# Performance work log

Measured on AMD Instinct MI355X. Metric: run time of the kernel, lower is better.

## Reference

```python
import jax, jax.numpy as jnp
import numpy as np

# Constants matching init_kwargs
N_HEADS = 8
D_MODEL = 256
PATCH_NUM = 128
D_K = D_MODEL // N_HEADS  # 32
TEMP = 0.5
EPS = 1e-10


def setup_inputs() -> dict:
    key = jax.random.key(0)
    ks = jax.random.split(key, 20)
    s = 0.02
    d, h, n = D_MODEL, N_HEADS, PATCH_NUM
    inp = {
        "x": jax.random.normal(ks[0], (32, n, d), dtype=jnp.float32),
        "gumbel_u": jax.random.uniform(ks[1], (h, n, n, 2), dtype=jnp.float32),
        "memory_w": jax.random.normal(ks[2], (n, h * d), dtype=jnp.float32) * s,
        "fc_out_w": jax.random.normal(ks[3], (2 * d, d), dtype=jnp.float32) * s,
        "fc_out_b": jnp.zeros((d,), jnp.float32),
        "fc_cat_w": jax.random.normal(ks[4], (d, 2), dtype=jnp.float32) * s,
        "fc_cat_b": jnp.zeros((2,), jnp.float32),
        "wq": jax.random.normal(ks[5], (d, d), dtype=jnp.float32) * s,
        "bq": jnp.zeros((d,), jnp.float32),
        "wk": jax.random.normal(ks[6], (d, d), dtype=jnp.float32) * s,
        "bk": jnp.zeros((d,), jnp.float32),
        "wv": jax.random.normal(ks[7], (d, d), dtype=jnp.float32) * s,
        "bv": jnp.zeros((d,), jnp.float32),
        "out_w": jax.random.normal(ks[8], (d, d), dtype=jnp.float32) * s,
        "out_b": jnp.zeros((d,), jnp.float32),
        "mlp_w1": jax.random.normal(ks[9], (d, d), dtype=jnp.float32) * s,
        "mlp_b1": jnp.zeros((d,), jnp.float32),
        "mlp_w2": jax.random.normal(ks[10], (d, d), dtype=jnp.float32) * s,
        "mlp_b2": jnp.zeros((d,), jnp.float32),
    }
    return inp


def _forward(x, memory_w, fc_out_w, fc_out_b, fc_cat_w, fc_cat_b,
             wq, bq, wk, bk, wv, bv, out_w, out_b,
             mlp_w1, mlp_b1, mlp_w2, mlp_b2, gumbel_u):
    H, N, D = N_HEADS, PATCH_NUM, D_MODEL
    B = x.shape[0]

    # ---- SSConnectionLearning on memory feats ----
    # memory: Embedding(N, d_model*n_heads) -> feats [H, N, D]
    feats = memory_w.reshape(N, H, D).transpose(1, 0, 2)
    # rel_rec gathers row index i (receiver), rel_send gathers col index j (sender)
    senders = jnp.broadcast_to(feats[:, None, :, :], (H, N, N, D))   # feats[j]
    receivers = jnp.broadcast_to(feats[:, :, None, :], (H, N, N, D))  # feats[i]
    pair = jnp.concatenate([senders, receivers], axis=-1)  # [H,N,N,2D]
    hdn = jax.nn.relu(jnp.einsum('hijc,cd->hijd', pair, fc_out_w) + fc_out_b)
    logits = jnp.einsum('hijd,dk->hijk', hdn, fc_cat_w) + fc_cat_b  # [H,N,N,2]

    # gumbel-softmax, hard=True, straight-through
    g = -jnp.log(-jnp.log(gumbel_u + EPS) + EPS)
    y_soft = jax.nn.softmax((logits + g) / TEMP, axis=-1)
    y_hard = jax.nn.one_hot(jnp.argmax(y_soft, axis=-1), 2, dtype=y_soft.dtype)
    y = jax.lax.stop_gradient(y_hard - y_soft) + y_soft
    conn = y[..., 1]  # [H,N,N] learned sparse connection mask

    # ---- PatchIntegration (GELU MLP, dropout = identity in eval) ----
    xm = jax.nn.gelu(x @ mlp_w1 + mlp_b1)
    xm = xm @ mlp_w2 + mlp_b2

    # ---- Multihead attention masked by connection matrix ----
    q = (xm @ wq + bq).reshape(B, N, H, D_K).transpose(0, 2, 1, 3)  # [B,H,N,dk]
    k = (xm @ wk + bk).reshape(B, N, H, D_K).transpose(0, 2, 1, 3)
    v = (xm @ wv + bv).reshape(B, N, H, D_K).transpose(0, 2, 1, 3)
    scale = D_K ** -0.5
    scores = jnp.einsum('bhqd,bhkd->bhqk', q, k) * scale
    # additive mask: blocked where conn==0 (large negative keeps softmax finite)
    scores = scores + (conn[None] - 1.0) * 1e9
    attn = jax.nn.softmax(scores, axis=-1)
    out = jnp.einsum('bhqk,bhkd->bhqd', attn, v)
    out = out.transpose(0, 2, 1, 3).reshape(B, N, H * D_K)
    out = out @ out_w + out_b
    return out


def reference(x, gumbel_u, memory_w, fc_out_w, fc_out_b, fc_cat_w, fc_cat_b,
              wq, bq, wk, bk, wv, bv, out_w, out_b,
              mlp_w1, mlp_b1, mlp_w2, mlp_b2):
    return _forward(x, memory_w, fc_out_w, fc_out_b, fc_cat_w, fc_cat_b,
                    wq, bq, wk, bk, wv, bv, out_w, out_b,
                    mlp_w1, mlp_b1, mlp_w2, mlp_b2, gumbel_u)
```

## Files before the change

kernel.cpp:

```cpp
#include <hip/hip_runtime.h>
#include <hip/hip_bf16.h>
#include <math.h>


typedef short short8 __attribute__((ext_vector_type(8)));
typedef float f32x4 __attribute__((ext_vector_type(4)));

union V8 { uint4 u; short8 s; };

__device__ __forceinline__ float gelu_f(float x) {
    float inner = 0.7978845608028654f * (x + 0.044715f * x * x * x);
    return 0.5f * x * (1.0f + tanhf(inner));
}
__device__ __forceinline__ void split_bf16(float x, ushort& h, ushort& l) {
    __hip_bfloat16 bh = __float2bfloat16(x);
    float hf = __bfloat162float(bh);
    __hip_bfloat16 bl = __float2bfloat16(x - hf);
    h = __builtin_bit_cast(ushort, bh);
    l = __builtin_bit_cast(ushort, bl);
}
__device__ __forceinline__ ushort bf16bits(float x) {
    return __builtin_bit_cast(ushort, __float2bfloat16(x));
}
__device__ __forceinline__ float bits_to_f(ushort v) {
    return __builtin_bit_cast(float, ((uint)v) << 16);
}
__device__ __forceinline__ short8 lds_frag(const ushort* p) {
    V8 v; v.u = *(const uint4*)p; return v.s;
}

__global__ __launch_bounds__(256) void k_wprep(
    const float* __restrict__ w0, const float* __restrict__ w1,
    const float* __restrict__ w2, const float* __restrict__ w3,
    const float* __restrict__ w4, const float* __restrict__ w5,
    const float* __restrict__ w6, const float* __restrict__ w7,
    ushort* __restrict__ hi, ushort* __restrict__ lo) {
    int bx = blockIdx.x;
    int m = bx >> 4, ks = (bx >> 1) & 7, nh = bx & 1;
    const float* W = m == 0 ? w0 : m == 1 ? w1 : m == 2 ? w2 : m == 3 ? w3 :
                     m == 4 ? w4 : m == 5 ? w5 : m == 6 ? w6 : w7;
    ushort* Hm = hi + m * 65536;
    ushort* Lm = lo + m * 65536;
    __shared__ __align__(16) float xs[32 * 132];
    int t = threadIdx.x;
    #pragma unroll
    for (int p = 0; p < 4; ++p) {
        int idx = p * 256 + t;
        int row = idx >> 5, c4 = (idx & 31) * 4;
        *(float4*)(xs + row * 132 + c4) =
            *(const float4*)(W + (ks * 32 + row) * 256 + nh * 128 + c4);
    }
    __syncthreads();
    int lane = t & 63, lr = lane & 15, quad = lane >> 4;
    #pragma unroll
    for (int it = 0; it < 2; ++it) {
        int tgl = (t >> 6) + 4 * it;
        int tg = nh * 8 + tgl;
        int nl = tgl * 16 + lr;
        ushort hb[8], lb[8];
        #pragma unroll
        for (int j = 0; j < 8; ++j)
            split_bf16(xs[(quad * 8 + j) * 132 + nl], hb[j], lb[j]);
        uint4 ph = { (uint)hb[0] | ((uint)hb[1] << 16), (uint)hb[2] | ((uint)hb[3] << 16),
                     (uint)hb[4] | ((uint)hb[5] << 16), (uint)hb[6] | ((uint)hb[7] << 16) };
        uint4 pl = { (uint)lb[0] | ((uint)lb[1] << 16), (uint)lb[2] | ((uint)lb[3] << 16),
                     (uint)lb[4] | ((uint)lb[5] << 16), (uint)lb[6] | ((uint)lb[7] << 16) };
        int idx = ((tg * 8 + ks) * 64 + lane) * 8;
        *(uint4*)(Hm + idx) = ph;
        *(uint4*)(Lm + idx) = pl;
    }
}

__global__ __launch_bounds__(256) void k_featproj(
    const float* __restrict__ memory_w,
    const ushort* __restrict__ Whi, const ushort* __restrict__ Wlo,
    float* __restrict__ A, float* __restrict__ Bm) {
    __shared__ __align__(16) ushort xhi[16 * 264], xlo[16 * 264];
    int t = threadIdx.x;
    int rt = blockIdx.x;
    int msel = blockIdx.y & 1, cq = blockIdx.y >> 1;
    #pragma unroll
    for (int ii = 0; ii < 4; ++ii) {
        int f4 = ii * 256 + t;
        int rr = f4 >> 6, c = (f4 & 63) * 4;
        int r = rt * 16 + rr;
        int h = r >> 7, n = r & 127;
        float4 xv = *(const float4*)(memory_w + n * 2048 + h * 256 + c);
        ushort hh[4], ll[4];
        split_bf16(xv.x, hh[0], ll[0]); split_bf16(xv.y, hh[1], ll[1]);
        split_bf16(xv.z, hh[2], ll[2]); split_bf16(xv.w, hh[3], ll[3]);
        uint2 ph = { (uint)hh[0] | ((uint)hh[1] << 16), (uint)hh[2] | ((uint)hh[3] << 16) };
        uint2 pl = { (uint)ll[0] | ((uint)ll[1] << 16), (uint)ll[2] | ((uint)ll[3] << 16) };
        *(uint2*)(xhi + rr * 264 + c) = ph;
        *(uint2*)(xlo + rr * 264 + c) = pl;
    }
    __syncthreads();
    int l = t & 63, w = t >> 6;
    int lr = l & 15, quad = l >> 4;
    int tg = cq * 4 + w;
    const uint4* H4 = (const uint4*)(Whi + (6 + msel) * 65536);
    const uint4* L4 = (const uint4*)(Wlo + (6 + msel) * 65536);
    const ushort* ah = xhi + lr * 264 + quad * 8;
    const ushort* al = xlo + lr * 264 + quad * 8;
    f32x4 acc = {};
    #pragma unroll
    for (int ks = 0; ks < 8; ++ks) {
        short8 a_h = lds_frag(ah + ks * 32);
        short8 a_l = lds_frag(al + ks * 32);
        int off = (tg * 8 + ks) * 64 + l;
        V8 bh, bl; bh.u = H4[off]; bl.u = L4[off];
        acc = __builtin_amdgcn_mfma_f32_16x16x32_bf16(a_h, bh.s, acc, 0, 0, 0);
        acc = __builtin_amdgcn_mfma_f32_16x16x32_bf16(a_l, bh.s, acc, 0, 0, 0);
        acc = __builtin_amdgcn_mfma_f32_16x16x32_bf16(a_h, bl.s, acc, 0, 0, 0);
    }
    float* O = msel ? Bm : A;
    int n0 = tg * 16 + lr;
    #pragma unroll
    for (int r = 0; r < 4; ++r)
        O[(rt * 16 + quad * 4 + r) * 256 + n0] = acc[r];
}

__global__ __launch_bounds__(256) void k_conn(
    const float* __restrict__ A, const float* __restrict__ Bm,
    const float* __restrict__ fc_out_b, const float* __restrict__ fc_cat_w,
    const float* __restrict__ fc_cat_b, const float* __restrict__ gumbel_u,
    ushort* __restrict__ maskb) {
    int bx = blockIdx.x;
    int h = bx >> 6, it = (bx >> 3) & 7, jt = bx & 7;
    int i0 = it * 16, j0 = jt * 16;
    int t = threadIdx.x;
    int il = t >> 4, jl = t & 15;
    __shared__ __align__(16) float sA[16 * 260], sB[16 * 260];
    #pragma unroll
    for (int p = 0; p < 4; ++p) {
        int idx = p * 256 + t;
        int rr = idx >> 6, c = (idx & 63) * 4;
        *(float4*)(sA + rr * 260 + c) =
            *(const float4*)(A + (h * 128 + j0 + rr) * 256 + c);
        float4 bv = *(const float4*)(Bm + (h * 128 + i0 + rr) * 256 + c);
        float4 fb = *(const float4*)(fc_out_b + c);
        bv.x += fb.x; bv.y += fb.y; bv.z += fb.z; bv.w += fb.w;
        *(float4*)(sB + rr * 260 + c) = bv;
    }
    __syncthreads();
    const float* Ar = sA + jl * 260;
    const float* Br = sB + il * 260;
    float l0 = fc_cat_b[0], l1 = fc_cat_b[1];
    #pragma unroll 4
    for (int d4 = 0; d4 < 64; ++d4) {
        int d = d4 * 4;
        float4 av = *(const float4*)(Ar + d);
        float4 bv = *(const float4*)(Br + d);
        float4 cwA = *(const float4*)(fc_cat_w + d * 2);
        float4 cwB = *(const float4*)(fc_cat_w + d * 2 + 4);
        float h0 = fmaxf(av.x + bv.x, 0.f);
        float h1 = fmaxf(av.y + bv.y, 0.f);
        float h2 = fmaxf(av.z + bv.z, 0.f);
        float h3 = fmaxf(av.w + bv.w, 0.f);
        l0 += h0 * cwA.x + h1 * cwA.z + h2 * cwB.x + h3 * cwB.z;
        l1 += h0 * cwA.y + h1 * cwA.w + h2 * cwB.y + h3 * cwB.w;
    }
    int i = i0 + il, j = j0 + jl;
    float2 uu = *(const float2*)(gumbel_u + ((h * 128 + i) * 128 + j) * 2);
    float g0 = -logf(-logf(uu.x + 1e-10f) + 1e-10f);
    float g1 = -logf(-logf(uu.y + 1e-10f) + 1e-10f);
    bool on = (l1 + g1) > (l0 + g0);
    maskb[(h * 128 + i) * 128 + j] = bf16bits(on ? 0.f : -1e9f);
}

__global__ __launch_bounds__(512) void k_fused3(
    const float* __restrict__ X,
    const ushort* __restrict__ Whi, const ushort* __restrict__ Wlo,
    const float* __restrict__ b1, const float* __restrict__ b2,
    const float* __restrict__ Bq, const float* __restrict__ Bk,
    const float* __restrict__ Bv,
    ushort* __restrict__ Q, ushort* __restrict__ K, ushort* __restrict__ V) {
    __shared__ __align__(16) ushort aHi[16 * 264], aLo[16 * 264];
    __shared__ __align__(16) ushort bHi[16 * 264], bLo[16 * 264];
    int t = threadIdx.x;
    int r0 = blockIdx.x * 16;
    #pragma unroll
    for (int ii = 0; ii < 2; ++ii) {
        int f4 = ii * 512 + t;
        int row = f4 >> 6, c = (f4 & 63) * 4;
        float4 xv = *(const float4*)(X + (r0 + row) * 256 + c);
        ushort h[4], l[4];
        split_bf16(xv.x, h[0], l[0]); split_bf16(xv.y, h[1], l[1]);
        split_bf16(xv.z, h[2], l[2]); split_bf16(xv.w, h[3], l[3]);
        uint2 ph = { (uint)h[0] | ((uint)h[1] << 16), (uint)h[2] | ((uint)h[3] << 16) };
        uint2 pl = { (uint)l[0] | ((uint)l[1] << 16), (uint)l[2] | ((uint)l[3] << 16) };
        *(uint2*)(aHi + row * 264 + c) = ph;
        *(uint2*)(aLo + row * 264 + c) = pl;
    }
    __syncthreads();
    int lane = t & 63, w = t >> 6;
    int lr = lane & 15, quad = lane >> 4;
    int aoff = lr * 264 + quad * 8;
    {
        const uint4* H4 = (const uint4*)(Whi + 0 * 65536);
        const uint4* L4 = (const uint4*)(Wlo + 0 * 65536);
        f32x4 acc[2] = {};
        #pragma unroll
        for (int ks = 0; ks < 8; ++ks) {
            short8 a_h = lds_frag(aHi + aoff + ks * 32);
            short8 a_l = lds_frag(aLo + aoff + ks * 32);
            #pragma unroll
            for (int ti = 0; ti < 2; ++ti) {
                int off = ((w * 2 + ti) * 8 + ks) * 64 + lane;
                V8 bh, bl; bh.u = H4[off]; bl.u = L4[off];
                acc[ti] = __builtin_amdgcn_mfma_f32_16x16x32_bf16(a_h, bh.s, acc[ti], 0, 0, 0);
                acc[ti] = __builtin_amdgcn_mfma_f32_16x16x32_bf16(a_l, bh.s, acc[ti], 0, 0, 0);
                acc[ti] = __builtin_amdgcn_mfma_f32_16x16x32_bf16(a_h, bl.s, acc[ti], 0, 0, 0);
            }
        }
        #pragma unroll
        for (int ti = 0; ti < 2; ++ti) {
            int n0 = (w * 2 + ti) * 16 + lr;
            float bb = b1[n0];
            #pragma unroll
            for (int r = 0; r < 4; ++r) {
                float o = gelu_f(acc[ti][r] + bb);
                ushort hh, ll; split_bf16(o, hh, ll);
                int ad = (quad * 4 + r) * 264 + n0;
                bHi[ad] = hh; bLo[ad] = ll;
            }
        }
    }
    __syncthreads();
    {
        const uint4* H4 = (const uint4*)(Whi + 1 * 65536);
        const uint4* L4 = (const uint4*)(Wlo + 1 * 65536);
        f32x4 acc[2] = {};
        #pragma unroll
        for (int ks = 0; ks < 8; ++ks) {
            short8 a_h = lds_frag(bHi + aoff + ks * 32);
            short8 a_l = lds_frag(bLo + aoff + ks * 32);
            #pragma unroll
            for (int ti = 0; ti < 2; ++ti) {
                int off = ((w * 2 + ti) * 8 + ks) * 64 + lane;
                V8 bh, bl; bh.u = H4[off]; bl.u = L4[off];
                acc[ti] = __builtin_amdgcn_mfma_f32_16x16x32_bf16(a_h, bh.s, acc[ti], 0, 0, 0);
                acc[ti] = __builtin_amdgcn_mfma_f32_16x16x32_bf16(a_l, bh.s, acc[ti], 0, 0, 0);
                acc[ti] = __builtin_amdgcn_mfma_f32_16x16x32_bf16(a_h, bl.s, acc[ti], 0, 0, 0);
            }
        }
        __syncthreads();
        #pragma unroll
        for (int ti = 0; ti < 2; ++ti) {
            int n0 = (w * 2 + ti) * 16 + lr;
            float bb = b2[n0];
            #pragma unroll
            for (int r = 0; r < 4; ++r) {
                float o = acc[ti][r] + bb;
                ushort hh, ll; split_bf16(o, hh, ll);
                int ad = (quad * 4 + r) * 264 + n0;
                aHi[ad] = hh; aLo[ad] = ll;
            }
        }
    }
    __syncthreads();
    {
        const uint4* Hq = (const uint4*)(Whi + 2 * 65536);
        const uint4* Lq = (const uint4*)(Wlo + 2 * 65536);
        const uint4* Hk = (const uint4*)(Whi + 3 * 65536);
        const uint4* Lk = (const uint4*)(Wlo + 3 * 65536);
        const uint4* Hv = (const uint4*)(Whi + 4 * 65536);
        const uint4* Lv = (const uint4*)(Wlo + 4 * 65536);
        f32x4 aq[2] = {}, ak[2] = {}, av[2] = {};
        #pragma unroll 2
        for (int ks = 0; ks < 8; ++ks) {
            short8 a_h = lds_frag(aHi + aoff + ks * 32);
            short8 a_l = lds_frag(aLo + aoff + ks * 32);
            #pragma unroll
            for (int ti = 0; ti < 2; ++ti) {
                int off = ((w * 2 + ti) * 8 + ks) * 64 + lane;
                V8 qh, ql, kh, kl, vh, vl;
                qh.u = Hq[off]; ql.u = Lq[off];
                kh.u = Hk[off]; kl.u = Lk[off];
                vh.u = Hv[off]; vl.u = Lv[off];
                aq[ti] = __builtin_amdgcn_mfma_f32_16x16x32_bf16(a_h, qh.s, aq[ti], 0, 0, 0);
                aq[ti] = __builtin_amdgcn_mfma_f32_16x16x32_bf16(a_l, qh.s, aq[ti], 0, 0, 0);
                aq[ti] = __builtin_amdgcn_mfma_f32_16x16x32_bf16(a_h, ql.s, aq[ti], 0, 0, 0);
                ak[ti] = __builtin_amdgcn_mfma_f32_16x16x32_bf16(a_h, kh.s, ak[ti], 0, 0, 0);
                ak[ti] = __builtin_amdgcn_mfma_f32_16x16x32_bf16(a_l, kh.s, ak[ti], 0, 0, 0);
                ak[ti] = __builtin_amdgcn_mfma_f32_16x16x32_bf16(a_h, kl.s, ak[ti], 0, 0, 0);
                av[ti] = __builtin_amdgcn_mfma_f32_16x16x32_bf16(a_h, vh.s, av[ti], 0, 0, 0);
                av[ti] = __builtin_amdgcn_mfma_f32_16x16x32_bf16(a_l, vh.s, av[ti], 0, 0, 0);
                av[ti] = __builtin_amdgcn_mfma_f32_16x16x32_bf16(a_h, vl.s, av[ti], 0, 0, 0);
            }
        }
        #pragma unroll
        for (int ti = 0; ti < 2; ++ti) {
            int n0 = (w * 2 + ti) * 16 + lr;
            float bq = Bq[n0], bk = Bk[n0], bv = Bv[n0];
            #pragma unroll
            for (int r = 0; r < 4; ++r) {
                int go = (r0 + quad * 4 + r) * 256 + n0;
                Q[go] = bf16bits(aq[ti][r] + bq);
                K[go] = bf16bits(ak[ti][r] + bk);
                V[go] = bf16bits(av[ti][r] + bv);
            }
        }
    }
}

__global__ __launch_bounds__(256) void k_attn_mfma(
    const ushort* __restrict__ Q, const ushort* __restrict__ K,
    const ushort* __restrict__ V, const ushort* __restrict__ maskb,
    float* __restrict__ AO) {
    int bx = blockIdx.x;
    int b = bx >> 4, h = (bx >> 1) & 7, rh = bx & 1;
    int t = threadIdx.x;
    int lane = t & 63, w = t >> 6;
    __shared__ __align__(16) ushort vT[32 * 136];
    __shared__ __align__(16) ushort ps[64 * 136];
    #pragma unroll
    for (int it = 0; it < 2; ++it) {
        int idx = it * 256 + t;
        int key = idx >> 2, dq8 = (idx & 3) * 8;
        V8 vv; vv.u = *(const uint4*)(V + (b * 128 + key) * 256 + h * 32 + dq8);
        #pragma unroll
        for (int m = 0; m < 8; ++m)
            vT[(dq8 + m) * 136 + key] = (ushort)vv.s[m];
    }
    __syncthreads();
    int lr = lane & 15, quad = lane >> 4;
    int rt = rh * 4 + w;
    V8 af;
    af.u = *(const uint4*)(Q + (b * 128 + rt * 16 + lr) * 256 + h * 32 + quad * 8);
    f32x4 s[8];
    #pragma unroll
    for (int ct = 0; ct < 8; ++ct) {
        V8 bf_;
        bf_.u = *(const uint4*)(K + (b * 128 + ct * 16 + lr) * 256 + h * 32 + quad * 8);
        f32x4 z = {0.f, 0.f, 0.f, 0.f};
        s[ct] = __builtin_amdgcn_mfma_f32_16x16x32_bf16(af.s, bf_.s, z, 0, 0, 0);
    }
    const float scale = 0.17677669529663687f;
    const ushort* mrow = maskb + h * 16384;
    #pragma unroll
    for (int r = 0; r < 4; ++r) {
        int lrow = w * 16 + quad * 4 + r;
        int grow = rt * 16 + quad * 4 + r;
        float sv[8];
        float mx = -3.0e38f;
        #pragma unroll
        for (int ct = 0; ct < 8; ++ct) {
            float bias = bits_to_f(mrow[grow * 128 + ct * 16 + lr]);
            sv[ct] = s[ct][r] * scale + bias;
            mx = fmaxf(mx, sv[ct]);
        }
        mx = fmaxf(mx, __shfl_xor(mx, 1));
        mx = fmaxf(mx, __shfl_xor(mx, 2));
        mx = fmaxf(mx, __shfl_xor(mx, 4));
        mx = fmaxf(mx, __shfl_xor(mx, 8));
        float sum = 0.f;
        #pragma unroll
        for (int ct = 0; ct < 8; ++ct) {
            sv[ct] = __expf(sv[ct] - mx);
            sum += sv[ct];
        }
        sum += __shfl_xor(sum, 1);
        sum += __shfl_xor(sum, 2);
        sum += __shfl_xor(sum, 4);
        sum += __shfl_xor(sum, 8);
        float iv = 1.f / sum;
        #pragma unroll
        for (int ct = 0; ct < 8; ++ct)
            ps[lrow * 136 + ct * 16 + lr] = bf16bits(sv[ct] * iv);
    }
    f32x4 o0 = {}, o1 = {};
    #pragma unroll
    for (int kk = 0; kk < 4; ++kk) {
        short8 pa = lds_frag(ps + (w * 16 + lr) * 136 + kk * 32 + quad * 8);
        short8 v0 = lds_frag(vT + lr * 136 + kk * 32 + quad * 8);
        short8 v1 = lds_frag(vT + (16 + lr) * 136 + kk * 32 + quad * 8);
        o0 = __builtin_amdgcn_mfma_f32_16x16x32_bf16(pa, v0, o0, 0, 0, 0);
        o1 = __builtin_amdgcn_mfma_f32_16x16x32_bf16(pa, v1, o1, 0, 0, 0);
    }
    #pragma unroll
    for (int r = 0; r < 4; ++r) {
        int grow = rt * 16 + quad * 4 + r;
        float* op = AO + b * 32768 + grow * 256 + h * 32;
        op[lr] = o0[r];
        op[16 + lr] = o1[r];
    }
}

__global__ __launch_bounds__(256) void k_gemm16(
    const float* __restrict__ X, const ushort* __restrict__ Whi,
    const ushort* __restrict__ Wlo, const float* __restrict__ bias,
    float* __restrict__ Y) {
    __shared__ __align__(16) ushort xhi[16 * 264], xlo[16 * 264];
    int t = threadIdx.x;
    int r0 = blockIdx.x * 16;
    #pragma unroll
    for (int ii = 0; ii < 4; ++ii) {
        int f4 = ii * 256 + t;
        int row = f4 >> 6, c = (f4 & 63) * 4;
        float4 xv = *(const float4*)(X + (r0 + row) * 256 + c);
        ushort h[4], l[4];
        split_bf16(xv.x, h[0], l[0]); split_bf16(xv.y, h[1], l[1]);
        split_bf16(xv.z, h[2], l[2]); split_bf16(xv.w, h[3], l[3]);
        uint2 ph = { (uint)h[0] | ((uint)h[1] << 16), (uint)h[2] | ((uint)h[3] << 16) };
        uint2 pl = { (uint)l[0] | ((uint)l[1] << 16), (uint)l[2] | ((uint)l[3] << 16) };
        *(uint2*)(xhi + row * 264 + c) = ph;
        *(uint2*)(xlo + row * 264 + c) = pl;
    }
    __syncthreads();
    int l = t & 63, w = t >> 6;
    int lr = l & 15, quad = l >> 4;
    int tg = blockIdx.y * 4 + w;
    const ushort* ah = xhi + lr * 264 + quad * 8;
    const ushort* al = xlo + lr * 264 + quad * 8;
    const uint4* H4 = (const uint4*)Whi;
    const uint4* L4 = (const uint4*)Wlo;
    f32x4 acc = {};
    #pragma unroll
    for (int ks = 0; ks < 8; ++ks) {
        short8 a_h = lds_frag(ah + ks * 32);
        short8 a_l = lds_frag(al + ks * 32);
        int off = (tg * 8 + ks) * 64 + l;
        V8 bh, bl; bh.u = H4[off]; bl.u = L4[off];
        acc = __builtin_amdgcn_mfma_f32_16x16x32_bf16(a_h, bh.s, acc, 0, 0, 0);
        acc = __builtin_amdgcn_mfma_f32_16x16x32_bf16(a_l, bh.s, acc, 0, 0, 0);
        acc = __builtin_amdgcn_mfma_f32_16x16x32_bf16(a_h, bl.s, acc, 0, 0, 0);
    }
    int n0 = tg * 16 + lr;
    float bs = bias[n0];
    #pragma unroll
    for (int r = 0; r < 4; ++r)
        Y[(r0 + quad * 4 + r) * 256 + n0] = acc[r] + bs;
}

extern "C" void kernel_launch(void* const* d_in, const int* in_sizes, int n_in,
                              void* d_out, int out_size, void* d_ws, size_t ws_size,
                              hipStream_t stream) {
    const float* x        = (const float*)d_in[0];
    const float* gumbel_u = (const float*)d_in[1];
    const float* memory_w = (const float*)d_in[2];
    const float* fc_out_w = (const float*)d_in[3];
    const float* fc_out_b = (const float*)d_in[4];
    const float* fc_cat_w = (const float*)d_in[5];
    const float* fc_cat_b = (const float*)d_in[6];
    const float* wq       = (const float*)d_in[7];
    const float* bq       = (const float*)d_in[8];
    const float* wk       = (const float*)d_in[9];
    const float* bk       = (const float*)d_in[10];
    const float* wv_      = (const float*)d_in[11];
    const float* bv_      = (const float*)d_in[12];
    const float* out_w    = (const float*)d_in[13];
    const float* out_b    = (const float*)d_in[14];
    const float* mlp_w1   = (const float*)d_in[15];
    const float* mlp_b1   = (const float*)d_in[16];
    const float* mlp_w2   = (const float*)d_in[17];
    const float* mlp_b2   = (const float*)d_in[18];

    float* ws    = (float*)d_ws;
    float* A     = ws;
    float* Bm    = ws + 262144;
    ushort* mask = (ushort*)(ws + 524288);
    ushort* qb   = (ushort*)(ws + 589824);
    ushort* kb   = (ushort*)(ws + 1114112);
    ushort* vb   = (ushort*)(ws + 1638400);
    float* ao    = ws + 2162688;
    ushort* wf_hi = (ushort*)(ws + 3211264);
    ushort* wf_lo = wf_hi + 8 * 65536;
    float* out   = (float*)d_out;

    k_wprep<<<dim3(128), dim3(256), 0, stream>>>(
        mlp_w1, mlp_w2, wq, wk, wv_, out_w, fc_out_w, fc_out_w + 65536,
        wf_hi, wf_lo);
    k_featproj<<<dim3(64, 8), dim3(256), 0, stream>>>(memory_w, wf_hi, wf_lo, A, Bm);
    k_fused3<<<dim3(256), dim3(512), 0, stream>>>(x, wf_hi, wf_lo, mlp_b1, mlp_b2,
                                                  bq, bk, bv_, qb, kb, vb);
    k_conn<<<dim3(512), dim3(256), 0, stream>>>(A, Bm, fc_out_b, fc_cat_w, fc_cat_b,
                                                gumbel_u, mask);
    k_attn_mfma<<<dim3(512), dim3(256), 0, stream>>>(qb, kb, vb, mask, ao);
    k_gemm16<<<dim3(256, 4), dim3(256), 0, stream>>>(ao, wf_hi + 5 * 65536,
                                                     wf_lo + 5 * 65536, out_b, out);
}
```

Baseline: 159.2 us.

## Merge feature projection and MLP/QKV kernels into one launch, widen blocks

Combines the memory-feature projection kernel and the fused MLP+QKV kernel into a single launch, with the block index choosing the work: 64 blocks do the feature projection and 256 blocks do the MLP+QKV path. This removes one kernel launch and lets the two independent stages run at the same time. The weight-prep and connection kernels switch to 512-thread blocks that each handle twice the work, halving their grid sizes. The risks are load imbalance between the two block types, since the feature blocks now loop over four column tiles each, and lower occupancy from the larger blocks.

New measurement: 144.7 us (median of 2 runs). 1.1x faster.

```diff
diff --git a/kernel.cpp b/kernel.cpp
--- a/kernel.cpp
+++ b/kernel.cpp
@@ -29,32 +29,36 @@
     V8 v; v.u = *(const uint4*)p; return v.s;
 }
 
-__global__ __launch_bounds__(256) void k_wprep(
-    const float* __restrict__ w0, const float* __restrict__ w1,
-    const float* __restrict__ w2, const float* __restrict__ w3,
-    const float* __restrict__ w4, const float* __restrict__ w5,
-    const float* __restrict__ w6, const float* __restrict__ w7,
+
+__global__ __launch_bounds__(512) void k_wprep(
+    const float* __restrict__ mlp_w1, const float* __restrict__ mlp_w2,
+    const float* __restrict__ wq, const float* __restrict__ wk,
+    const float* __restrict__ wv, const float* __restrict__ out_w,
+    const float* __restrict__ fc_out_w,
     ushort* __restrict__ hi, ushort* __restrict__ lo) {
-    int bx = blockIdx.x;
-    int m = bx >> 4, ks = (bx >> 1) & 7, nh = bx & 1;
-    const float* W = m == 0 ? w0 : m == 1 ? w1 : m == 2 ? w2 : m == 3 ? w3 :
-                     m == 4 ? w4 : m == 5 ? w5 : m == 6 ? w6 : w7;
+    __shared__ __align__(16) float xs2[2][32 * 132];
+    int bx = blockIdx.x, t = threadIdx.x;
+    int half = t >> 8, tl = t & 255;
+    int job = bx * 2 + half;
+    int m = job >> 4, ks = (job >> 1) & 7, nh = job & 1;
+    const float* W = m == 0 ? mlp_w1 : m == 1 ? mlp_w2 : m == 2 ? wq :
+                     m == 3 ? wk : m == 4 ? wv : m == 5 ? out_w :
+                     m == 6 ? fc_out_w : fc_out_w + 65536;
     ushort* Hm = hi + m * 65536;
     ushort* Lm = lo + m * 65536;
-    __shared__ __align__(16) float xs[32 * 132];
-    int t = threadIdx.x;
+    float* xs = xs2[half];
     #pragma unroll
     for (int p = 0; p < 4; ++p) {
-        int idx = p * 256 + t;
+        int idx = p * 256 + tl;
         int row = idx >> 5, c4 = (idx & 31) * 4;
         *(float4*)(xs + row * 132 + c4) =
             *(const float4*)(W + (ks * 32 + row) * 256 + nh * 128 + c4);
     }
     __syncthreads();
-    int lane = t & 63, lr = lane & 15, quad = lane >> 4;
+    int lane = tl & 63, lr = lane & 15, quad = lane >> 4;
     #pragma unroll
     for (int it = 0; it < 2; ++it) {
-        int tgl = (t >> 6) + 4 * it;
+        int tgl = (tl >> 6) + 4 * it;
         int tg = nh * 8 + tgl;
         int nl = tgl * 16 + lr;
         ushort hb[8], lb[8];
@@ -71,76 +75,222 @@
     }
 }
 
-__global__ __launch_bounds__(256) void k_featproj(
-    const float* __restrict__ memory_w,
+__global__ __launch_bounds__(512) void k_p2(
+    const float* __restrict__ memory_w, const float* __restrict__ X,
     const ushort* __restrict__ Whi, const ushort* __restrict__ Wlo,
-    float* __restrict__ A, float* __restrict__ Bm) {
-    __shared__ __align__(16) ushort xhi[16 * 264], xlo[16 * 264];
-    int t = threadIdx.x;
-    int rt = blockIdx.x;
-    int msel = blockIdx.y & 1, cq = blockIdx.y >> 1;
-    #pragma unroll
-    for (int ii = 0; ii < 4; ++ii) {
-        int f4 = ii * 256 + t;
-        int rr = f4 >> 6, c = (f4 & 63) * 4;
-        int r = rt * 16 + rr;
-        int h = r >> 7, n = r & 127;
-        float4 xv = *(const float4*)(memory_w + n * 2048 + h * 256 + c);
-        ushort hh[4], ll[4];
-        split_bf16(xv.x, hh[0], ll[0]); split_bf16(xv.y, hh[1], ll[1]);
-        split_bf16(xv.z, hh[2], ll[2]); split_bf16(xv.w, hh[3], ll[3]);
-        uint2 ph = { (uint)hh[0] | ((uint)hh[1] << 16), (uint)hh[2] | ((uint)hh[3] << 16) };
-        uint2 pl = { (uint)ll[0] | ((uint)ll[1] << 16), (uint)ll[2] | ((uint)ll[3] << 16) };
-        *(uint2*)(xhi + rr * 264 + c) = ph;
-        *(uint2*)(xlo + rr * 264 + c) = pl;
-    }
-    __syncthreads();
-    int l = t & 63, w = t >> 6;
-    int lr = l & 15, quad = l >> 4;
-    int tg = cq * 4 + w;
-    const uint4* H4 = (const uint4*)(Whi + (6 + msel) * 65536);
-    const uint4* L4 = (const uint4*)(Wlo + (6 + msel) * 65536);
-    const ushort* ah = xhi + lr * 264 + quad * 8;
-    const ushort* al = xlo + lr * 264 + quad * 8;
-    f32x4 acc = {};
-    #pragma unroll
-    for (int ks = 0; ks < 8; ++ks) {
-        short8 a_h = lds_frag(ah + ks * 32);
-        short8 a_l = lds_frag(al + ks * 32);
-        int off = (tg * 8 + ks) * 64 + l;
-        V8 bh, bl; bh.u = H4[off]; bl.u = L4[off];
-        acc = __builtin_amdgcn_mfma_f32_16x16x32_bf16(a_h, bh.s, acc, 0, 0, 0);
-        acc = __builtin_amdgcn_mfma_f32_16x16x32_bf16(a_l, bh.s, acc, 0, 0, 0);
-        acc = __builtin_amdgcn_mfma_f32_16x16x32_bf16(a_h, bl.s, acc, 0, 0, 0);
-    }
-    float* O = msel ? Bm : A;
-    int n0 = tg * 16 + lr;
-    #pragma unroll
-    for (int r = 0; r < 4; ++r)
-        O[(rt * 16 + quad * 4 + r) * 256 + n0] = acc[r];
-}
-
-__global__ __launch_bounds__(256) void k_conn(
-    const float* __restrict__ A, const float* __restrict__ Bm,
+    const float* __restrict__ b1, const float* __restrict__ b2,
+    const float* __restrict__ Bq, const float* __restrict__ Bk,
+    const float* __restrict__ Bv,
+    float* __restrict__ A, float* __restrict__ Bm,
+    ushort* __restrict__ Q, ushort* __restrict__ K, ushort* __restrict__ V) {
+    __shared__ __align__(16) union {
+        struct { ushort xhi[16 * 264], xlo[16 * 264]; } f;
+        struct {
+            ushort aHi[16 * 264], aLo[16 * 264];
+            ushort bHi[16 * 264], bLo[16 * 264];
+        } g;
+    } sm;
+    int bx = blockIdx.x, t = threadIdx.x;
+    if (bx < 64) {
+        int rt = bx;
+        #pragma unroll
+        for (int ii = 0; ii < 2; ++ii) {
+            int f4 = ii * 512 + t;
+            int rr = f4 >> 6, c = (f4 & 63) * 4;
+            int r = rt * 16 + rr;
+            int h = r >> 7, n = r & 127;
+            float4 xv = *(const float4*)(memory_w + n * 2048 + h * 256 + c);
+            ushort hh[4], ll[4];
+            split_bf16(xv.x, hh[0], ll[0]); split_bf16(xv.y, hh[1], ll[1]);
+            split_bf16(xv.z, hh[2], ll[2]); split_bf16(xv.w, hh[3], ll[3]);
+            uint2 ph = { (uint)hh[0] | ((uint)hh[1] << 16), (uint)hh[2] | ((uint)hh[3] << 16) };
+            uint2 pl = { (uint)ll[0] | ((uint)ll[1] << 16), (uint)ll[2] | ((uint)ll[3] << 16) };
+            *(uint2*)(sm.f.xhi + rr * 264 + c) = ph;
+            *(uint2*)(sm.f.xlo + rr * 264 + c) = pl;
+        }
+        __syncthreads();
+        int lane = t & 63, w = t >> 6;
+        int lr = lane & 15, quad = lane >> 4;
+        int msel = w & 1, cq = w >> 1;
+        const uint4* H4 = (const uint4*)(Whi + (6 + msel) * 65536);
+        const uint4* L4 = (const uint4*)(Wlo + (6 + msel) * 65536);
+        const ushort* ah = sm.f.xhi + lr * 264 + quad * 8;
+        const ushort* al = sm.f.xlo + lr * 264 + quad * 8;
+        float* O = msel ? Bm : A;
+        #pragma unroll
+        for (int i = 0; i < 4; ++i) {
+            int tg = cq * 4 + i;
+            f32x4 acc = {};
+            #pragma unroll
+            for (int ks = 0; ks < 8; ++ks) {
+                short8 a_h = lds_frag(ah + ks * 32);
+                short8 a_l = lds_frag(al + ks * 32);
+                int off = (tg * 8 + ks) * 64 + lane;
+                V8 bh, bl; bh.u = H4[off]; bl.u = L4[off];
+                acc = __builtin_amdgcn_mfma_f32_16x16x32_bf16(a_h, bh.s, acc, 0, 0, 0);
+                acc = __builtin_amdgcn_mfma_f32_16x16x32_bf16(a_l, bh.s, acc, 0, 0, 0);
+                acc = __builtin_amdgcn_mfma_f32_16x16x32_bf16(a_h, bl.s, acc, 0, 0, 0);
+            }
+            int n0 = tg * 16 + lr;
+            #pragma unroll
+            for (int r = 0; r < 4; ++r)
+                O[(rt * 16 + quad * 4 + r) * 256 + n0] = acc[r];
+        }
+        return;
+    }
+    int r0 = (bx - 64) * 16;
+    #pragma unroll
+    for (int ii = 0; ii < 2; ++ii) {
+        int f4 = ii * 512 + t;
+        int row = f4 >> 6, c = (f4 & 63) * 4;
+        float4 xv = *(const float4*)(X + (r0 + row) * 256 + c);
+        ushort h[4], l[4];
+        split_bf16(xv.x, h[0], l[0]); split_bf16(xv.y, h[1], l[1]);
+        split_bf16(xv.z, h[2], l[2]); split_bf16(xv.w, h[3], l[3]);
+        uint2 ph = { (uint)h[0] | ((uint)h[1] << 16), (uint)h[2] | ((uint)h[3] << 16) };
+        uint2 pl = { (uint)l[0] | ((uint)l[1] << 16), (uint)l[2] | ((uint)l[3] << 16) };
+        *(uint2*)(sm.g.aHi + row * 264 + c) = ph;
+        *(uint2*)(sm.g.aLo + row * 264 + c) = pl;
+    }
+    __syncthreads();
+    int lane = t & 63, w = t >> 6;
+    int lr = lane & 15, quad = lane >> 4;
+    int aoff = lr * 264 + quad * 8;
+    {
+        const uint4* H4 = (const uint4*)(Whi + 0 * 65536);
+        const uint4* L4 = (const uint4*)(Wlo + 0 * 65536);
+        f32x4 acc[2] = {};
+        #pragma unroll
+        for (int ks = 0; ks < 8; ++ks) {
+            short8 a_h = lds_frag(sm.g.aHi + aoff + ks * 32);
+            short8 a_l = lds_frag(sm.g.aLo + aoff + ks * 32);
+            #pragma unroll
+            for (int ti = 0; ti < 2; ++ti) {
+                int off = ((w * 2 + ti) * 8 + ks) * 64 + lane;
+                V8 bh, bl; bh.u = H4[off]; bl.u = L4[off];
+                acc[ti] = __builtin_amdgcn_mfma_f32_16x16x32_bf16(a_h, bh.s, acc[ti], 0, 0, 0);
+                acc[ti] = __builtin_amdgcn_mfma_f32_16x16x32_bf16(a_l, bh.s, acc[ti], 0, 0, 0);
+                acc[ti] = __builtin_amdgcn_mfma_f32_16x16x32_bf16(a_h, bl.s, acc[ti], 0, 0, 0);
+            }
+        }
+        #pragma unroll
+        for (int ti = 0; ti < 2; ++ti) {
+            int n0 = (w * 2 + ti) * 16 + lr;
+            float bb = b1[n0];
+            #pragma unroll
+            for (int r = 0; r < 4; ++r) {
+                float o = gelu_f(acc[ti][r] + bb);
+                ushort hh, ll; split_bf16(o, hh, ll);
+                int ad = (quad * 4 + r) * 264 + n0;
+                sm.g.bHi[ad] = hh; sm.g.bLo[ad] = ll;
+            }
+        }
+    }
+    __syncthreads();
+    {
+        const uint4* H4 = (const uint4*)(Whi + 1 * 65536);
+        const uint4* L4 = (const uint4*)(Wlo + 1 * 65536);
+        f32x4 acc[2] = {};
+        #pragma unroll
+        for (int ks = 0; ks < 8; ++ks) {
+            short8 a_h = lds_frag(sm.g.bHi + aoff + ks * 32);
+            short8 a_l = lds_frag(sm.g.bLo + aoff + ks * 32);
+            #pragma unroll
+            for (int ti = 0; ti < 2; ++ti) {
+                int off = ((w * 2 + ti) * 8 + ks) * 64 + lane;
+                V8 bh, bl; bh.u = H4[off]; bl.u = L4[off];
+                acc[ti] = __builtin_amdgcn_mfma_f32_16x16x32_bf16(a_h, bh.s, acc[ti], 0, 0, 0);
+                acc[ti] = __builtin_amdgcn_mfma_f32_16x16x32_bf16(a_l, bh.s, acc[ti], 0, 0, 0);
+                acc[ti] = __builtin_amdgcn_mfma_f32_16x16x32_bf16(a_h, bl.s, acc[ti], 0, 0, 0);
+            }
+        }
+        __syncthreads();
+        #pragma unroll
+        for (int ti = 0; ti < 2; ++ti) {
+            int n0 = (w * 2 + ti) * 16 + lr;
+            float bb = b2[n0];
+            #pragma unroll
+            for (int r = 0; r < 4; ++r) {
+                float o = acc[ti][r] + bb;
+                ushort hh, ll; split_bf16(o, hh, ll);
+                int ad = (quad * 4 + r) * 264 + n0;
+                sm.g.aHi[ad] = hh; sm.g.aLo[ad] = ll;
+            }
+        }
+    }
+    __syncthreads();
+    {
+        const uint4* Hq = (const uint4*)(Whi + 2 * 65536);
+        const uint4* Lq = (const uint4*)(Wlo + 2 * 65536);
+        const uint4* Hk = (const uint4*)(Whi + 3 * 65536);
+        const uint4* Lk = (const uint4*)(Wlo + 3 * 65536);
+        const uint4* Hv = (const uint4*)(Whi + 4 * 65536);
+        const uint4* Lv = (const uint4*)(Wlo + 4 * 65536);
+        f32x4 aq[2] = {}, ak[2] = {}, av[2] = {};
+        #pragma unroll 2
+        for (int ks = 0; ks < 8; ++ks) {
+            short8 a_h = lds_frag(sm.g.aHi + aoff + ks * 32);
+            short8 a_l = lds_frag(sm.g.aLo + aoff + ks * 32);
+            #pragma unroll
+            for (int ti = 0; ti < 2; ++ti) {
+                int off = ((w * 2 + ti) * 8 + ks) * 64 + lane;
+                V8 qh, ql, kh, kl, vh, vl;
+                qh.u = Hq[off]; ql.u = Lq[off];
+                kh.u = Hk[off]; kl.u = Lk[off];
+                vh.u = Hv[off]; vl.u = Lv[off];
+                aq[ti] = __builtin_amdgcn_mfma_f32_16x16x32_bf16(a_h, qh.s, aq[ti], 0, 0, 0);
+                aq[ti] = __builtin_amdgcn_mfma_f32_16x16x32_bf16(a_l, qh.s, aq[ti], 0, 0, 0);
+                aq[ti] = __builtin_amdgcn_mfma_f32_16x16x32_bf16(a_h, ql.s, aq[ti], 0, 0, 0);
+                ak[ti] = __builtin_amdgcn_mfma_f32_16x16x32_bf16(a_h, kh.s, ak[ti], 0, 0, 0);
+                ak[ti] = __builtin_amdgcn_mfma_f32_16x16x32_bf16(a_l, kh.s, ak[ti], 0, 0, 0);
+                ak[ti] = __builtin_amdgcn_mfma_f32_16x16x32_bf16(a_h, kl.s, ak[ti], 0, 0, 0);
+                av[ti] = __builtin_amdgcn_mfma_f32_16x16x32_bf16(a_h, vh.s, av[ti], 0, 0, 0);
+                av[ti] = __builtin_amdgcn_mfma_f32_16x16x32_bf16(a_l, vh.s, av[ti], 0, 0, 0);
+                av[ti] = __builtin_amdgcn_mfma_f32_16x16x32_bf16(a_h, vl.s, av[ti], 0, 0, 0);
+            }
+        }
+        #pragma unroll
+        for (int ti = 0; ti < 2; ++ti) {
+            int n0 = (w * 2 + ti) * 16 + lr;
+            float bq = Bq[n0], bk = Bk[n0], bv = Bv[n0];
+            #pragma unroll
+            for (int r = 0; r < 4; ++r) {
+                int go = (r0 + quad * 4 + r) * 256 + n0;
+                Q[go] = bf16bits(aq[ti][r] + bq);
+                K[go] = bf16bits(ak[ti][r] + bk);
+                V[go] = bf16bits(av[ti][r] + bv);
+            }
+        }
+    }
+}
+
+__global__ __launch_bounds__(512) void k_conn(
+    const float* __restrict__ A, const float* __restrict__ Bmat,
     const float* __restrict__ fc_out_b, const float* __restrict__ fc_cat_w,
     const float* __restrict__ fc_cat_b, const float* __restrict__ gumbel_u,
     ushort* __restrict__ maskb) {
-    int bx = blockIdx.x;
-    int h = bx >> 6, it = (bx >> 3) & 7, jt = bx & 7;
-    int i0 = it * 16, j0 = jt * 16;
-    int t = threadIdx.x;
-    int il = t >> 4, jl = t & 15;
-    __shared__ __align__(16) float sA[16 * 260], sB[16 * 260];
-    #pragma unroll
-    for (int p = 0; p < 4; ++p) {
-        int idx = p * 256 + t;
-        int rr = idx >> 6, c = (idx & 63) * 4;
-        *(float4*)(sA + rr * 260 + c) =
-            *(const float4*)(A + (h * 128 + j0 + rr) * 256 + c);
-        float4 bv = *(const float4*)(Bm + (h * 128 + i0 + rr) * 256 + c);
-        float4 fb = *(const float4*)(fc_out_b + c);
-        bv.x += fb.x; bv.y += fb.y; bv.z += fb.z; bv.w += fb.w;
-        *(float4*)(sB + rr * 260 + c) = bv;
+    __shared__ __align__(16) float sA[16 * 260], sB[32 * 260];
+    int bx = blockIdx.x, t = threadIdx.x;
+    int h = bx >> 5;
+    int rem = bx & 31;
+    int it = rem >> 3, jt = rem & 7;
+    int i0 = it * 32, j0 = jt * 16;
+    int jl = t & 15, il = t >> 4;
+    #pragma unroll
+    for (int p = 0; p < 6; ++p) {
+        int id2 = p * 512 + t;
+        if (id2 < 1024) {
+            int rr = id2 >> 6, c = (id2 & 63) * 4;
+            *(float4*)(sA + rr * 260 + c) =
+                *(const float4*)(A + (h * 128 + j0 + rr) * 256 + c);
+        } else {
+            int id3 = id2 - 1024;
+            int rr = id3 >> 6, c = (id3 & 63) * 4;
+            float4 bv = *(const float4*)(Bmat + (h * 128 + i0 + rr) * 256 + c);
+            float4 fb = *(const float4*)(fc_out_b + c);
+            bv.x += fb.x; bv.y += fb.y; bv.z += fb.z; bv.w += fb.w;
+            *(float4*)(sB + rr * 260 + c) = bv;
+        }
     }
     __syncthreads();
     const float* Ar = sA + jl * 260;
@@ -166,142 +316,6 @@
     float g1 = -logf(-logf(uu.y + 1e-10f) + 1e-10f);
     bool on = (l1 + g1) > (l0 + g0);
     maskb[(h * 128 + i) * 128 + j] = bf16bits(on ? 0.f : -1e9f);
-}
-
-__global__ __launch_bounds__(512) void k_fused3(
-    const float* __restrict__ X,
-    const ushort* __restrict__ Whi, const ushort* __restrict__ Wlo,
-    const float* __restrict__ b1, const float* __restrict__ b2,
-    const float* __restrict__ Bq, const float* __restrict__ Bk,
-    const float* __restrict__ Bv,
-    ushort* __restrict__ Q, ushort* __restrict__ K, ushort* __restrict__ V) {
-    __shared__ __align__(16) ushort aHi[16 * 264], aLo[16 * 264];
-    __shared__ __align__(16) ushort bHi[16 * 264], bLo[16 * 264];
-    int t = threadIdx.x;
-    int r0 = blockIdx.x * 16;
-    #pragma unroll
-    for (int ii = 0; ii < 2; ++ii) {
-        int f4 = ii * 512 + t;
-        int row = f4 >> 6, c = (f4 & 63) * 4;
-        float4 xv = *(const float4*)(X + (r0 + row) * 256 + c);
-        ushort h[4], l[4];
-        split_bf16(xv.x, h[0], l[0]); split_bf16(xv.y, h[1], l[1]);
-        split_bf16(xv.z, h[2], l[2]); split_bf16(xv.w, h[3], l[3]);
-        uint2 ph = { (uint)h[0] | ((uint)h[1] << 16), (uint)h[2] | ((uint)h[3] << 16) };
-        uint2 pl = { (uint)l[0] | ((uint)l[1] << 16), (uint)l[2] | ((uint)l[3] << 16) };
-        *(uint2*)(aHi + row * 264 + c) = ph;
-        *(uint2*)(aLo + row * 264 + c) = pl;
-    }
-    __syncthreads();
-    int lane = t & 63, w = t >> 6;
-    int lr = lane & 15, quad = lane >> 4;
-    int aoff = lr * 264 + quad * 8;
-    {
-        const uint4* H4 = (const uint4*)(Whi + 0 * 65536);
-        const uint4* L4 = (const uint4*)(Wlo + 0 * 65536);
-        f32x4 acc[2] = {};
-        #pragma unroll
-        for (int ks = 0; ks < 8; ++ks) {
-            short8 a_h = lds_frag(aHi + aoff + ks * 32);
-            short8 a_l = lds_frag(aLo + aoff + ks * 32);
-            #pragma unroll
-            for (int ti = 0; ti < 2; ++ti) {
-                int off = ((w * 2 + ti) * 8 + ks) * 64 + lane;
-                V8 bh, bl; bh.u = H4[off]; bl.u = L4[off];
-                acc[ti] = __builtin_amdgcn_mfma_f32_16x16x32_bf16(a_h, bh.s, acc[ti], 0, 0, 0);
-                acc[ti] = __builtin_amdgcn_mfma_f32_16x16x32_bf16(a_l, bh.s, acc[ti], 0, 0, 0);
-                acc[ti] = __builtin_amdgcn_mfma_f32_16x16x32_bf16(a_h, bl.s, acc[ti], 0, 0, 0);
-            }
-        }
-        #pragma unroll
-        for (int ti = 0; ti < 2; ++ti) {
-            int n0 = (w * 2 + ti) * 16 + lr;
-            float bb = b1[n0];
-            #pragma unroll
-            for (int r = 0; r < 4; ++r) {
-                float o = gelu_f(acc[ti][r] + bb);
-                ushort hh, ll; split_bf16(o, hh, ll);
-                int ad = (quad * 4 + r) * 264 + n0;
-                bHi[ad] = hh; bLo[ad] = ll;
-            }
-        }
-    }
-    __syncthreads();
-    {
-        const uint4* H4 = (const uint4*)(Whi + 1 * 65536);
-        const uint4* L4 = (const uint4*)(Wlo + 1 * 65536);
-        f32x4 acc[2] = {};
-        #pragma unroll
-        for (int ks = 0; ks < 8; ++ks) {
-            short8 a_h = lds_frag(bHi + aoff + ks * 32);
-            short8 a_l = lds_frag(bLo + aoff + ks * 32);
-            #pragma unroll
-            for (int ti = 0; ti < 2; ++ti) {
-                int off = ((w * 2 + ti) * 8 + ks) * 64 + lane;
-                V8 bh, bl; bh.u = H4[off]; bl.u = L4[off];
-                acc[ti] = __builtin_amdgcn_mfma_f32_16x16x32_bf16(a_h, bh.s, acc[ti], 0, 0, 0);
-                acc[ti] = __builtin_amdgcn_mfma_f32_16x16x32_bf16(a_l, bh.s, acc[ti], 0, 0, 0);
-                acc[ti] = __builtin_amdgcn_mfma_f32_16x16x32_bf16(a_h, bl.s, acc[ti], 0, 0, 0);
-            }
-        }
-        __syncthreads();
-        #pragma unroll
-        for (int ti = 0; ti < 2; ++ti) {
-            int n0 = (w * 2 + ti) * 16 + lr;
-            float bb = b2[n0];
-            #pragma unroll
-            for (int r = 0; r < 4; ++r) {
-                float o = acc[ti][r] + bb;
-                ushort hh, ll; split_bf16(o, hh, ll);
-                int ad = (quad * 4 + r) * 264 + n0;
-                aHi[ad] = hh; aLo[ad] = ll;
-            }
-        }
-    }
-    __syncthreads();
-    {
-        const uint4* Hq = (const uint4*)(Whi + 2 * 65536);
-        const uint4* Lq = (const uint4*)(Wlo + 2 * 65536);
-        const uint4* Hk = (const uint4*)(Whi + 3 * 65536);
-        const uint4* Lk = (const uint4*)(Wlo + 3 * 65536);
-        const uint4* Hv = (const uint4*)(Whi + 4 * 65536);
-        const uint4* Lv = (const uint4*)(Wlo + 4 * 65536);
-        f32x4 aq[2] = {}, ak[2] = {}, av[2] = {};
-        #pragma unroll 2
-        for (int ks = 0; ks < 8; ++ks) {
-            short8 a_h = lds_frag(aHi + aoff + ks * 32);
-            short8 a_l = lds_frag(aLo + aoff + ks * 32);
-            #pragma unroll
-            for (int ti = 0; ti < 2; ++ti) {
-                int off = ((w * 2 + ti) * 8 + ks) * 64 + lane;
-                V8 qh, ql, kh, kl, vh, vl;
-                qh.u = Hq[off]; ql.u = Lq[off];
-                kh.u = Hk[off]; kl.u = Lk[off];
-                vh.u = Hv[off]; vl.u = Lv[off];
-                aq[ti] = __builtin_amdgcn_mfma_f32_16x16x32_bf16(a_h, qh.s, aq[ti], 0, 0, 0);
-                aq[ti] = __builtin_amdgcn_mfma_f32_16x16x32_bf16(a_l, qh.s, aq[ti], 0, 0, 0);
-                aq[ti] = __builtin_amdgcn_mfma_f32_16x16x32_bf16(a_h, ql.s, aq[ti], 0, 0, 0);
-                ak[ti] = __builtin_amdgcn_mfma_f32_16x16x32_bf16(a_h, kh.s, ak[ti], 0, 0, 0);
-                ak[ti] = __builtin_amdgcn_mfma_f32_16x16x32_bf16(a_l, kh.s, ak[ti], 0, 0, 0);
-                ak[ti] = __builtin_amdgcn_mfma_f32_16x16x32_bf16(a_h, kl.s, ak[ti], 0, 0, 0);
-                av[ti] = __builtin_amdgcn_mfma_f32_16x16x32_bf16(a_h, vh.s, av[ti], 0, 0, 0);
-                av[ti] = __builtin_amdgcn_mfma_f32_16x16x32_bf16(a_l, vh.s, av[ti], 0, 0, 0);
-                av[ti] = __builtin_amdgcn_mfma_f32_16x16x32_bf16(a_h, vl.s, av[ti], 0, 0, 0);
-            }
-        }
-        #pragma unroll
-        for (int ti = 0; ti < 2; ++ti) {
-            int n0 = (w * 2 + ti) * 16 + lr;
-            float bq = Bq[n0], bk = Bk[n0], bv = Bv[n0];
-            #pragma unroll
-            for (int r = 0; r < 4; ++r) {
-                int go = (r0 + quad * 4 + r) * 256 + n0;
-                Q[go] = bf16bits(aq[ti][r] + bq);
-                K[go] = bf16bits(ak[ti][r] + bk);
-                V[go] = bf16bits(av[ti][r] + bv);
-            }
-        }
-    }
 }
 
 __global__ __launch_bounds__(256) void k_attn_mfma(
@@ -468,14 +482,13 @@
     ushort* wf_lo = wf_hi + 8 * 65536;
     float* out   = (float*)d_out;
 
-    k_wprep<<<dim3(128), dim3(256), 0, stream>>>(
-        mlp_w1, mlp_w2, wq, wk, wv_, out_w, fc_out_w, fc_out_w + 65536,
-        wf_hi, wf_lo);
-    k_featproj<<<dim3(64, 8), dim3(256), 0, stream>>>(memory_w, wf_hi, wf_lo, A, Bm);
-    k_fused3<<<dim3(256), dim3(512), 0, stream>>>(x, wf_hi, wf_lo, mlp_b1, mlp_b2,
-                                                  bq, bk, bv_, qb, kb, vb);
-    k_conn<<<dim3(512), dim3(256), 0, stream>>>(A, Bm, fc_out_b, fc_cat_w, fc_cat_b,
-                                                gumbel_u, mask);
+    k_wprep<<<dim3(64), dim3(512), 0, stream>>>(
+        mlp_w1, mlp_w2, wq, wk, wv_, out_w, fc_out_w, wf_hi, wf_lo);
+    k_p2<<<dim3(320), dim3(512), 0, stream>>>(
+        memory_w, x, wf_hi, wf_lo, mlp_b1, mlp_b2, bq, bk, bv_,
+        A, Bm, qb, kb, vb);
+    k_conn<<<dim3(256), dim3(512), 0, stream>>>(
+        A, Bm, fc_out_b, fc_cat_w, fc_cat_b, gumbel_u, mask);
     k_attn_mfma<<<dim3(512), dim3(256), 0, stream>>>(qb, kb, vb, mask, ao);
     k_gemm16<<<dim3(256, 4), dim3(256), 0, stream>>>(ao, wf_hi + 5 * 65536,
                                                      wf_lo + 5 * 65536, out_b, out);
```
